# Optimization experiments

Measured on AMD Instinct MI355X. Metric: run time of the kernel, lower is better.

Reference implementation:

```python
import jax, jax.numpy as jnp
import numpy as np
import math

B, S, DIM = 1, 2048, 1024
H, KVH = 16, 4
HD = DIM // H            # 64
KV_DIM = KVH * HD        # 256


def setup_inputs() -> dict:
    key = jax.random.key(0)
    ks = jax.random.split(key, 8)
    std = 0.02
    return {
        "x": jax.random.normal(ks[0], (B, S, DIM), jnp.float32),
        "Wq": jax.random.normal(ks[1], (DIM, DIM), jnp.float32) * std,
        "Wk": jax.random.normal(ks[2], (KV_DIM, DIM), jnp.float32) * std,
        "Wv": jax.random.normal(ks[3], (KV_DIM, DIM), jnp.float32) * std,
        "Wg": jax.random.normal(ks[4], (KV_DIM, DIM), jnp.float32) * std,
        "Wo": jax.random.normal(ks[5], (DIM, DIM), jnp.float32) * std,
        "q_gain": jnp.full((H,), 1.0, jnp.float32),
        "lambda_param": jnp.full((H,), 0.5, jnp.float32),
    }


def _rms_norm(x):
    eps = jnp.finfo(x.dtype).eps
    return x * jax.lax.rsqrt(jnp.mean(x * x, axis=-1, keepdims=True) + eps)


def _polar_rotary(seq_len, head_dim, dtype):
    # PolarRotary: angles = arange(0, d, 2)/d * pi; radius decays with position
    angles = jnp.arange(0, head_dim, 2, dtype=jnp.float32) / head_dim * math.pi
    pos = jnp.arange(seq_len, dtype=jnp.float32)
    radius = 1.0 / (1.0 + pos[:, None] * 0.01)          # [S, 1]
    ang = pos[:, None] * angles[None, :]                 # [S, d/2]
    cos = (radius * jnp.cos(ang)).astype(dtype)          # [S, d/2]
    sin = (radius * jnp.sin(ang)).astype(dtype)
    return cos[None, None], sin[None, None]              # [1,1,S,d/2]


def _apply_rotary(x, cos, sin):
    half = x.shape[-1] // 2
    x1, x2 = x[..., :half], x[..., half:]
    return jnp.concatenate([x1 * cos + x2 * sin, x1 * -sin + x2 * cos], axis=-1)


def _causal_attn(q, k, v, scale, mask):
    # q,k,v: [B,H,S,d]
    s = jnp.einsum("bhqd,bhkd->bhqk", q, k) * scale
    s = jnp.where(mask, s, jnp.finfo(s.dtype).min)
    p = jax.nn.softmax(s, axis=-1)
    return jnp.einsum("bhqk,bhkd->bhqd", p, v)


def reference(x, Wq, Wk, Wv, Wg, Wo, q_gain, lambda_param):
    bsz, seqlen, dim = x.shape
    q = (x @ Wq.T).reshape(bsz, seqlen, H, HD).transpose(0, 2, 1, 3)      # [B,H,S,d]
    k = (x @ Wk.T).reshape(bsz, seqlen, KVH, HD).transpose(0, 2, 1, 3)    # [B,KVH,S,d]
    v = (x @ Wv.T).reshape(bsz, seqlen, KVH, HD).transpose(0, 2, 1, 3)

    # value gate (VGA)
    v_g = jax.nn.sigmoid((x @ Wg.T).reshape(bsz, seqlen, KVH, HD).transpose(0, 2, 1, 3))
    v = v * v_g

    q = _rms_norm(q)
    k = _rms_norm(k)

    cos, sin = _polar_rotary(seqlen, HD, q.dtype)
    q = _apply_rotary(q, cos, sin)
    k = _apply_rotary(k, cos, sin)

    q = q * q_gain.astype(q.dtype)[None, :, None, None]

    # GQA: repeat kv heads
    rep = H // KVH
    k = jnp.repeat(k, rep, axis=1)
    v = jnp.repeat(v, rep, axis=1)

    # differential attention: split head dim in halves
    half = HD // 2
    q1, q2 = q[..., :half], q[..., half:]
    k1, k2 = k[..., :half], k[..., half:]
    v1, v2 = v[..., :half], v[..., half:]

    scale = 1.0 / math.sqrt(half)
    mask = jnp.tril(jnp.ones((seqlen, seqlen), dtype=bool))[None, None]
    a1 = _causal_attn(q1, k1, v1, scale, mask)
    a2 = _causal_attn(q2, k2, v2, scale, mask)

    lp = lambda_param.astype(q.dtype)[None, :, None, None]
    y = jnp.concatenate([a1 - lp * a2, a1 + lp * a2], axis=-1)            # [B,H,S,d]
    y = y.transpose(0, 2, 1, 3).reshape(bsz, seqlen, dim)
    return y @ Wo.T
```

## Files before the change

### kernel.cpp

```cpp
#include <hip/hip_runtime.h>
#include <hip/hip_bf16.h>
#include <math.h>

#define S_LEN 2048
#define DIM   1024
#define NH    16
#define NKVH  4
#define HD    64
#define KVDIM 256

typedef __hip_bfloat16 bf16;
typedef __attribute__((ext_vector_type(8))) short short8;
typedef __attribute__((ext_vector_type(4))) float f32x4;

#define GLOBAL_AS __attribute__((address_space(1)))
#define LDS_AS    __attribute__((address_space(3)))

__device__ __forceinline__ void gload_lds16(const bf16* g, bf16* l) {
    __builtin_amdgcn_global_load_lds((const GLOBAL_AS void*)g, (LDS_AS void*)l,
                                     16, 0, 0);
}

__global__ __launch_bounds__(256) void cast6(
    const float* __restrict__ x,  const float* __restrict__ Wq,
    const float* __restrict__ Wk, const float* __restrict__ Wv,
    const float* __restrict__ Wg, const float* __restrict__ Wo,
    bf16* __restrict__ xb,  bf16* __restrict__ Wqb,
    bf16* __restrict__ Wkb, bf16* __restrict__ Wvb,
    bf16* __restrict__ Wgb, bf16* __restrict__ Wob,
    float* __restrict__ rc, float* __restrict__ rs,
    const float* __restrict__ lp) {
    if (blockIdx.y == 6) {
        const int idx = blockIdx.x * 256 + threadIdx.x;
        if (idx < S_LEN * 32) {
            const int s = idx >> 5, i = idx & 31;
            float af  = (float)(((double)(2 * i) / 64.0) * 3.14159265358979323846);
            float ang = (float)s * af;
            float radius = 1.0f / (1.0f + 0.01f * (float)s);
            rc[idx] = radius * (float)cos((double)ang);
            rs[idx] = radius * (float)sin((double)ang);
        }
        return;
    }
    if (blockIdx.y == 5) {
        for (int i = (blockIdx.x * 256 + threadIdx.x) * 4; i < DIM * DIM;
             i += gridDim.x * 1024) {
            const int n = i >> 10, c = i & (DIM - 1);
            const int h = c >> 6, half = (c >> 5) & 1, d = c & 31;
            const float* base = Wo + (size_t)n * DIM + h * 64 + d;
            float4 w1 = *(const float4*)(base);
            float4 w2 = *(const float4*)(base + 32);
            const float lam = lp[h];
            float4 r;
            if (half == 0) {
                r.x = w1.x + w2.x; r.y = w1.y + w2.y;
                r.z = w1.z + w2.z; r.w = w1.w + w2.w;
            } else {
                r.x = lam * (w2.x - w1.x); r.y = lam * (w2.y - w1.y);
                r.z = lam * (w2.z - w1.z); r.w = lam * (w2.w - w1.w);
            }
            Wob[i]     = __float2bfloat16(r.x);
            Wob[i + 1] = __float2bfloat16(r.y);
            Wob[i + 2] = __float2bfloat16(r.z);
            Wob[i + 3] = __float2bfloat16(r.w);
        }
        return;
    }
    const float* s; bf16* d; int n;
    switch (blockIdx.y) {
        case 0: s = x;  d = xb;  n = S_LEN * DIM; break;
        case 1: s = Wq; d = Wqb; n = DIM * DIM;   break;
        case 2: s = Wk; d = Wkb; n = KVDIM * DIM; break;
        case 3: s = Wv; d = Wvb; n = KVDIM * DIM; break;
        default: s = Wg; d = Wgb; n = KVDIM * DIM; break;
    }
    for (int i = (blockIdx.x * 256 + threadIdx.x) * 4; i < n; i += gridDim.x * 1024) {
        float4 v = *(const float4*)(s + i);
        d[i]     = __float2bfloat16(v.x);
        d[i + 1] = __float2bfloat16(v.y);
        d[i + 2] = __float2bfloat16(v.z);
        d[i + 3] = __float2bfloat16(v.w);
    }
}

__device__ __forceinline__ void gemm_core(
    const bf16* __restrict__ A, const bf16* __restrict__ B,
    float* __restrict__ C, int bm, int bn, int N, int K) {
    __shared__ bf16 As[64 * 64];
    __shared__ bf16 Bs[64 * 64];
    const int tid  = threadIdx.x;
    const int w    = tid >> 6;
    const int lane = tid & 63;
    const int quad = lane >> 4;
    const int lm   = lane & 15;
    const int srow = tid >> 3;
    const int sseg = (tid & 7) ^ (srow & 7);
    const bf16* a0p = A + (size_t)(bm + srow) * K + (sseg << 3);
    const bf16* a1p = a0p + (size_t)32 * K;
    const bf16* b0p = B + (size_t)(bn + srow) * K + (sseg << 3);
    const bf16* b1p = b0p + (size_t)32 * K;
    bf16* ldsA = As + w * 512;
    bf16* ldsB = Bs + w * 512;

    f32x4 acc[4] = {};
    const int ra  = w * 16 + lm;
    const int rax = ra & 7;
    const int aoff0 = ra * 64 + (((quad    ) ^ rax) << 3);
    const int aoff1 = ra * 64 + (((quad + 4) ^ rax) << 3);
    const int rbx = lm & 7;
    const int boff0 = lm * 64 + (((quad    ) ^ rbx) << 3);
    const int boff1 = lm * 64 + (((quad + 4) ^ rbx) << 3);

    for (int k0 = 0; k0 < K; k0 += 64) {
        gload_lds16(a0p + k0, ldsA);
        gload_lds16(a1p + k0, ldsA + 2048);
        gload_lds16(b0p + k0, ldsB);
        gload_lds16(b1p + k0, ldsB + 2048);
        __syncthreads();
        short8 a0 = *(const short8*)&As[aoff0];
        short8 a1 = *(const short8*)&As[aoff1];
        #pragma unroll
        for (int t = 0; t < 4; ++t) {
            short8 b0 = *(const short8*)&Bs[boff0 + t * 16 * 64];
            short8 b1 = *(const short8*)&Bs[boff1 + t * 16 * 64];
            acc[t] = __builtin_amdgcn_mfma_f32_16x16x32_bf16(a0, b0, acc[t], 0, 0, 0);
            acc[t] = __builtin_amdgcn_mfma_f32_16x16x32_bf16(a1, b1, acc[t], 0, 0, 0);
        }
        __syncthreads();
    }
    const int r0 = bm + w * 16 + quad * 4;
    #pragma unroll
    for (int t = 0; t < 4; ++t) {
        const int col = bn + t * 16 + lm;
        #pragma unroll
        for (int i = 0; i < 4; ++i)
            C[(size_t)(r0 + i) * N + col] = acc[t][i];
    }
}

__global__ __launch_bounds__(256) void gemm_out(
    const bf16* __restrict__ Yb, const bf16* __restrict__ Wob,
    float* __restrict__ C) {
    gemm_core(Yb, Wob, C, blockIdx.y * 64, blockIdx.x * 64, DIM, DIM);
}

__global__ __launch_bounds__(256) void gemm_qkvg_post(
    const bf16* __restrict__ xb,  const bf16* __restrict__ Wqb,
    const bf16* __restrict__ Wkb, const bf16* __restrict__ Wvb,
    const bf16* __restrict__ Wgb,
    bf16* __restrict__ Qb, bf16* __restrict__ Kpk, bf16* __restrict__ Vpk,
    const float* __restrict__ qgain,
    const float* __restrict__ rc, const float* __restrict__ rs) {
    __shared__ bf16 As[64 * 64];
    __shared__ bf16 Bs[64 * 64];
    __shared__ bf16 Gs[64 * 64];
    const int cx = blockIdx.x;
    const int bm = blockIdx.y * 64;
    const int tid  = threadIdx.x;
    const int w    = tid >> 6;
    const int lane = tid & 63;
    const int quad = lane >> 4;
    const int lm   = lane & 15;
    const int srow = tid >> 3;
    const int sseg = (tid & 7) ^ (srow & 7);

    int mode, bn;
    const bf16 *B0, *B1;
    if (cx < 4)      { mode = 2; bn = cx * 64;        B0 = Wvb; B1 = Wgb; }
    else if (cx < 8) { mode = 1; bn = (cx - 4) * 64;  B0 = Wkb; B1 = Wkb; }
    else             { mode = 0; bn = (cx - 8) * 64;  B0 = Wqb; B1 = Wqb; }

    const bf16* a0p = xb + (size_t)(bm + srow) * DIM + (sseg << 3);
    const bf16* a1p = a0p + (size_t)32 * DIM;
    const bf16* b0p = B0 + (size_t)(bn + srow) * DIM + (sseg << 3);
    const bf16* b1p = b0p + (size_t)32 * DIM;
    const bf16* g0p = B1 + (size_t)(bn + srow) * DIM + (sseg << 3);
    const bf16* g1p = g0p + (size_t)32 * DIM;
    bf16* ldsA = As + w * 512;
    bf16* ldsB = Bs + w * 512;
    bf16* ldsG = Gs + w * 512;

    f32x4 acc[4]  = {};
    f32x4 acc2[4] = {};
    const int ra  = w * 16 + lm;
    const int rax = ra & 7;
    const int aoff0 = ra * 64 + (((quad    ) ^ rax) << 3);
    const int aoff1 = ra * 64 + (((quad + 4) ^ rax) << 3);
    const int rbx = lm & 7;
    const int boff0 = lm * 64 + (((quad    ) ^ rbx) << 3);
    const int boff1 = lm * 64 + (((quad + 4) ^ rbx) << 3);

    for (int k0 = 0; k0 < DIM; k0 += 64) {
        gload_lds16(a0p + k0, ldsA);
        gload_lds16(a1p + k0, ldsA + 2048);
        gload_lds16(b0p + k0, ldsB);
        gload_lds16(b1p + k0, ldsB + 2048);
        if (mode == 2) {
            gload_lds16(g0p + k0, ldsG);
            gload_lds16(g1p + k0, ldsG + 2048);
        }
        __syncthreads();
        short8 a0 = *(const short8*)&As[aoff0];
        short8 a1 = *(const short8*)&As[aoff1];
        #pragma unroll
        for (int t = 0; t < 4; ++t) {
            short8 b0 = *(const short8*)&Bs[boff0 + t * 16 * 64];
            short8 b1 = *(const short8*)&Bs[boff1 + t * 16 * 64];
            acc[t] = __builtin_amdgcn_mfma_f32_16x16x32_bf16(a0, b0, acc[t], 0, 0, 0);
            acc[t] = __builtin_amdgcn_mfma_f32_16x16x32_bf16(a1, b1, acc[t], 0, 0, 0);
        }
        if (mode == 2) {
            #pragma unroll
            for (int t = 0; t < 4; ++t) {
                short8 g0 = *(const short8*)&Gs[boff0 + t * 16 * 64];
                short8 g1 = *(const short8*)&Gs[boff1 + t * 16 * 64];
                acc2[t] = __builtin_amdgcn_mfma_f32_16x16x32_bf16(a0, g0, acc2[t], 0, 0, 0);
                acc2[t] = __builtin_amdgcn_mfma_f32_16x16x32_bf16(a1, g1, acc2[t], 0, 0, 0);
            }
        }
        __syncthreads();
    }

    const int r0 = bm + w * 16 + quad * 4;
    if (mode == 2) {
        const int kvh = cx;
        #pragma unroll
        for (int t = 0; t < 4; ++t) {
            const int d = t * 16 + lm;
            const int half = d >> 5, d32 = d & 31;
            #pragma unroll
            for (int i = 0; i < 4; ++i) {
                const int s = r0 + i;
                float val = acc[t][i] / (1.0f + __expf(-acc2[t][i]));
                const size_t vi = (((((size_t)(kvh*2 + half)*64 + (s>>5))*2 + (d32>>4))*64)
                                   + ((s&31)>>3)*16 + (d32&15))*8 + (s&7);
                Vpk[vi] = __float2bfloat16(val);
            }
        }
    } else {
        const float gain = (mode == 0) ? qgain[cx - 8] : 1.0f;
        float rr[4];
        #pragma unroll
        for (int i = 0; i < 4; ++i) {
            float v0 = acc[0][i] * acc[0][i] + acc[2][i] * acc[2][i];
            float v1 = acc[1][i] * acc[1][i] + acc[3][i] * acc[3][i];
            float ssv = v0 + v1;
            ssv += __shfl_xor(ssv, 8);
            ssv += __shfl_xor(ssv, 4);
            ssv += __shfl_xor(ssv, 2);
            ssv += __shfl_xor(ssv, 1);
            rr[i] = rsqrtf(ssv * (1.0f/64.0f) + 1.1920928955078125e-7f);
        }
        #pragma unroll
        for (int t = 0; t < 4; ++t) {
            const int d = t * 16 + lm;
            #pragma unroll
            for (int i = 0; i < 4; ++i) {
                const int s = r0 + i;
                float n  = acc[t][i]     * rr[i];
                float no = acc[t ^ 2][i] * rr[i];
                const int ri = s * 32 + (d & 31);
                float c = rc[ri], sn = rs[ri];
                float val = (t < 2) ? (n * c + no * sn) * gain
                                    : (n * c + -no * sn) * gain;
                if (mode == 0) {
                    Qb[(size_t)s * DIM + (cx - 8) * 64 + d] = __float2bfloat16(val);
                } else {
                    const int kvh = cx - 4;
                    const int half = d >> 5, d32 = d & 31;
                    const size_t ki = (((((size_t)(kvh*2 + half)*64 + (s>>5))*2 + ((s&31)>>4))*64)
                                       + (d32>>3)*16 + (s&15))*8 + (d32&7);
                    Kpk[ki] = __float2bfloat16(val);
                }
            }
        }
    }
}

__global__ __launch_bounds__(256, 8) void attn_mfma(
    const bf16* __restrict__ Qb, const bf16* __restrict__ Kpk,
    const bf16* __restrict__ Vpk, bf16* __restrict__ Yab) {
    __shared__ short PW[4][640];
    __shared__ float RED[3][64][13];
    const int id    = blockIdx.x;
    const int qtile = 127 - (id >> 5);
    const int hh    = id & 31;
    const int h     = hh >> 1;
    const int half  = hh & 1;
    const int kvh   = h >> 2;
    const int tid   = threadIdx.x;
    const int wid   = tid >> 6;
    const int lane  = tid & 63;
    const int quad  = lane >> 4;
    const int m     = lane & 15;
    bf16* PWb = (bf16*)PW[wid];

    const int qrow = qtile * 16 + m;
    short8 qf = *(const short8*)(Qb + (size_t)qrow * DIM + h * HD + half * 32 + quad * 8);

    const bf16* kbase = Kpk + (size_t)(kvh * 2 + half) * 64 * 1024 + lane * 8;
    const bf16* vbase = Vpk + (size_t)(kvh * 2 + half) * 64 * 1024 + lane * 8;

    f32x4 o0 = {}, o1 = {};
    float lpart[4] = {0.f, 0.f, 0.f, 0.f};
    const float scale = 0.17677669529663687f;
    const int rbase = qtile * 16 + quad * 4;
    const int nkt = (qtile >> 1) + 1;

    for (int kb = wid; kb < nkt; kb += 4) {
        short8 kf0 = *(const short8*)(kbase + kb * 1024);
        short8 kf1 = *(const short8*)(kbase + kb * 1024 + 512);
        f32x4 s0 = {}, s1 = {};
        s0 = __builtin_amdgcn_mfma_f32_16x16x32_bf16(qf, kf0, s0, 0, 0, 0);
        s1 = __builtin_amdgcn_mfma_f32_16x16x32_bf16(qf, kf1, s1, 0, 0, 0);
        short8 vt0 = *(const short8*)(vbase + kb * 1024);
        short8 vt1 = *(const short8*)(vbase + kb * 1024 + 512);
        const int kg = kb * 32 + m;
        #pragma unroll
        for (int r = 0; r < 4; ++r) {
            const int rg = rbase + r;
            const float p0 = (kg > rg)      ? 0.f : __expf(s0[r] * scale);
            const float p1 = (kg + 16 > rg) ? 0.f : __expf(s1[r] * scale);
            lpart[r] += p0 + p1;
            PWb[(quad * 4 + r) * 40 + m]      = __float2bfloat16(p0);
            PWb[(quad * 4 + r) * 40 + 16 + m] = __float2bfloat16(p1);
        }
        asm volatile("s_waitcnt lgkmcnt(0)" ::: "memory");
        short8 pf = *(const short8*)&PW[wid][m * 40 + quad * 8];
        o0 = __builtin_amdgcn_mfma_f32_16x16x32_bf16(pf, vt0, o0, 0, 0, 0);
        o1 = __builtin_amdgcn_mfma_f32_16x16x32_bf16(pf, vt1, o1, 0, 0, 0);
    }

    if (wid > 0) {
        float* rp = &RED[wid - 1][lane][0];
        #pragma unroll
        for (int r = 0; r < 4; ++r) {
            rp[r]     = o0[r];
            rp[4 + r] = o1[r];
            rp[8 + r] = lpart[r];
        }
    }
    __syncthreads();
    if (wid == 0) {
        #pragma unroll
        for (int wv = 0; wv < 3; ++wv) {
            const float* rp = &RED[wv][lane][0];
            #pragma unroll
            for (int r = 0; r < 4; ++r) {
                o0[r]     += rp[r];
                o1[r]     += rp[4 + r];
                lpart[r]  += rp[8 + r];
            }
        }
        #pragma unroll
        for (int r = 0; r < 4; ++r) {
            float v = lpart[r];
            v += __shfl_xor(v, 1);
            v += __shfl_xor(v, 2);
            v += __shfl_xor(v, 4);
            v += __shfl_xor(v, 8);
            lpart[r] = 1.f / v;
        }
        #pragma unroll
        for (int r = 0; r < 4; ++r) {
            bf16* op = Yab + (size_t)(rbase + r) * DIM + h * HD + half * 32;
            op[m]      = __float2bfloat16(o0[r] * lpart[r]);
            op[16 + m] = __float2bfloat16(o1[r] * lpart[r]);
        }
    }
}

extern "C" void kernel_launch(void* const* d_in, const int* in_sizes, int n_in,
                              void* d_out, int out_size, void* d_ws, size_t ws_size,
                              hipStream_t stream) {
    const float* x  = (const float*)d_in[0];
    const float* Wq = (const float*)d_in[1];
    const float* Wk = (const float*)d_in[2];
    const float* Wv = (const float*)d_in[3];
    const float* Wg = (const float*)d_in[4];
    const float* Wo = (const float*)d_in[5];
    const float* qg = (const float*)d_in[6];
    const float* lp = (const float*)d_in[7];
    float* out = (float*)d_out;

    char* ws = (char*)d_ws;
    bf16* Qb   = (bf16*)ws;
    bf16* Kpk  = (bf16*)(ws + (8u << 20));
    bf16* Vpk  = (bf16*)(ws + (9u << 20));
    float* rc  = (float*)(ws + (14u << 20));
    float* rs  = (float*)(ws + (14u << 20) + (256u << 10));
    bf16* Yab  = (bf16*)(ws + (14u << 20));
    bf16* xb   = (bf16*)(ws + (22u << 20));
    bf16* Wqb  = (bf16*)(ws + (26u << 20));
    bf16* Wkb  = (bf16*)(ws + (28u << 20));
    bf16* Wvb  = (bf16*)(ws + (28u << 20) + (512u << 10));
    bf16* Wgb  = (bf16*)(ws + (29u << 20));
    bf16* Wob  = (bf16*)(ws + (29u << 20) + (512u << 10));

    cast6<<<dim3(512, 7), 256, 0, stream>>>(x, Wq, Wk, Wv, Wg, Wo,
                                            xb, Wqb, Wkb, Wvb, Wgb, Wob,
                                            rc, rs, lp);

    gemm_qkvg_post<<<dim3(24, S_LEN/64), 256, 0, stream>>>(
        xb, Wqb, Wkb, Wvb, Wgb, Qb, Kpk, Vpk, qg, rc, rs);

    attn_mfma<<<4096, 256, 0, stream>>>(Qb, Kpk, Vpk, Yab);

    gemm_out<<<dim3(DIM/64, S_LEN/64), 256, 0, stream>>>(Yab, Wob, out);
}
```

Baseline: 131.1 us.

## Double-buffer LDS tiles in projection and output GEMMs

Both the fused QKVG projection GEMM and the output GEMM now keep two LDS buffers and prefetch the next K-tile with global-to-LDS loads while MFMAs consume the current tile. Each iteration ends with a single vmcnt wait and barrier instead of two __syncthreads. The goal is to hide global memory latency behind compute. In exchange LDS use doubles, which may lower occupancy, particularly in the projection kernel with its three buffers.

Result: no change. 133.0 us (+1.5%).

```diff
diff --git a/kernel.cpp b/kernel.cpp
--- a/kernel.cpp
+++ b/kernel.cpp
@@ -19,6 +19,12 @@
 __device__ __forceinline__ void gload_lds16(const bf16* g, bf16* l) {
     __builtin_amdgcn_global_load_lds((const GLOBAL_AS void*)g, (LDS_AS void*)l,
                                      16, 0, 0);
+}
+
+__device__ __forceinline__ void wait_stage_and_barrier() {
+    asm volatile("s_waitcnt vmcnt(0)" ::: "memory");
+    __builtin_amdgcn_s_barrier();
+    asm volatile("" ::: "memory");
 }
 
 __global__ __launch_bounds__(256) void cast6(
@@ -83,11 +89,11 @@
     }
 }
 
-__device__ __forceinline__ void gemm_core(
+__device__ __forceinline__ void gemm_core_db(
     const bf16* __restrict__ A, const bf16* __restrict__ B,
     float* __restrict__ C, int bm, int bn, int N, int K) {
-    __shared__ bf16 As[64 * 64];
-    __shared__ bf16 Bs[64 * 64];
+    __shared__ bf16 As[2][64 * 64];
+    __shared__ bf16 Bs[2][64 * 64];
     const int tid  = threadIdx.x;
     const int w    = tid >> 6;
     const int lane = tid & 63;
@@ -99,8 +105,7 @@
     const bf16* a1p = a0p + (size_t)32 * K;
     const bf16* b0p = B + (size_t)(bn + srow) * K + (sseg << 3);
     const bf16* b1p = b0p + (size_t)32 * K;
-    bf16* ldsA = As + w * 512;
-    bf16* ldsB = Bs + w * 512;
+    const int wo = w * 512;
 
     f32x4 acc[4] = {};
     const int ra  = w * 16 + lm;
@@ -111,22 +116,34 @@
     const int boff0 = lm * 64 + (((quad    ) ^ rbx) << 3);
     const int boff1 = lm * 64 + (((quad + 4) ^ rbx) << 3);
 
-    for (int k0 = 0; k0 < K; k0 += 64) {
-        gload_lds16(a0p + k0, ldsA);
-        gload_lds16(a1p + k0, ldsA + 2048);
-        gload_lds16(b0p + k0, ldsB);
-        gload_lds16(b1p + k0, ldsB + 2048);
-        __syncthreads();
-        short8 a0 = *(const short8*)&As[aoff0];
-        short8 a1 = *(const short8*)&As[aoff1];
-        #pragma unroll
-        for (int t = 0; t < 4; ++t) {
-            short8 b0 = *(const short8*)&Bs[boff0 + t * 16 * 64];
-            short8 b1 = *(const short8*)&Bs[boff1 + t * 16 * 64];
-            acc[t] = __builtin_amdgcn_mfma_f32_16x16x32_bf16(a0, b0, acc[t], 0, 0, 0);
-            acc[t] = __builtin_amdgcn_mfma_f32_16x16x32_bf16(a1, b1, acc[t], 0, 0, 0);
-        }
-        __syncthreads();
+    gload_lds16(a0p, &As[0][wo]);
+    gload_lds16(a1p, &As[0][wo] + 2048);
+    gload_lds16(b0p, &Bs[0][wo]);
+    gload_lds16(b1p, &Bs[0][wo] + 2048);
+    wait_stage_and_barrier();
+
+    const int nt = K >> 6;
+    #pragma unroll 2
+    for (int t = 0; t < nt; ++t) {
+        const int cur = t & 1;
+        if (t + 1 < nt) {
+            const int k0 = (t + 1) << 6;
+            const int nb = cur ^ 1;
+            gload_lds16(a0p + k0, &As[nb][wo]);
+            gload_lds16(a1p + k0, &As[nb][wo] + 2048);
+            gload_lds16(b0p + k0, &Bs[nb][wo]);
+            gload_lds16(b1p + k0, &Bs[nb][wo] + 2048);
+        }
+        short8 a0 = *(const short8*)&As[cur][aoff0];
+        short8 a1 = *(const short8*)&As[cur][aoff1];
+        #pragma unroll
+        for (int tt = 0; tt < 4; ++tt) {
+            short8 b0 = *(const short8*)&Bs[cur][boff0 + tt * 16 * 64];
+            short8 b1 = *(const short8*)&Bs[cur][boff1 + tt * 16 * 64];
+            acc[tt] = __builtin_amdgcn_mfma_f32_16x16x32_bf16(a0, b0, acc[tt], 0, 0, 0);
+            acc[tt] = __builtin_amdgcn_mfma_f32_16x16x32_bf16(a1, b1, acc[tt], 0, 0, 0);
+        }
+        if (t + 1 < nt) wait_stage_and_barrier();
     }
     const int r0 = bm + w * 16 + quad * 4;
     #pragma unroll
@@ -141,7 +158,7 @@
 __global__ __launch_bounds__(256) void gemm_out(
     const bf16* __restrict__ Yb, const bf16* __restrict__ Wob,
     float* __restrict__ C) {
-    gemm_core(Yb, Wob, C, blockIdx.y * 64, blockIdx.x * 64, DIM, DIM);
+    gemm_core_db(Yb, Wob, C, blockIdx.y * 64, blockIdx.x * 64, DIM, DIM);
 }
 
 __global__ __launch_bounds__(256) void gemm_qkvg_post(
@@ -151,9 +168,9 @@
     bf16* __restrict__ Qb, bf16* __restrict__ Kpk, bf16* __restrict__ Vpk,
     const float* __restrict__ qgain,
     const float* __restrict__ rc, const float* __restrict__ rs) {
-    __shared__ bf16 As[64 * 64];
-    __shared__ bf16 Bs[64 * 64];
-    __shared__ bf16 Gs[64 * 64];
+    __shared__ bf16 As[2][64 * 64];
+    __shared__ bf16 Bs[2][64 * 64];
+    __shared__ bf16 Gs[2][64 * 64];
     const int cx = blockIdx.x;
     const int bm = blockIdx.y * 64;
     const int tid  = threadIdx.x;
@@ -176,9 +193,7 @@
     const bf16* b1p = b0p + (size_t)32 * DIM;
     const bf16* g0p = B1 + (size_t)(bn + srow) * DIM + (sseg << 3);
     const bf16* g1p = g0p + (size_t)32 * DIM;
-    bf16* ldsA = As + w * 512;
-    bf16* ldsB = Bs + w * 512;
-    bf16* ldsG = Gs + w * 512;
+    const int wo = w * 512;
 
     f32x4 acc[4]  = {};
     f32x4 acc2[4] = {};
@@ -190,35 +205,51 @@
     const int boff0 = lm * 64 + (((quad    ) ^ rbx) << 3);
     const int boff1 = lm * 64 + (((quad + 4) ^ rbx) << 3);
 
-    for (int k0 = 0; k0 < DIM; k0 += 64) {
-        gload_lds16(a0p + k0, ldsA);
-        gload_lds16(a1p + k0, ldsA + 2048);
-        gload_lds16(b0p + k0, ldsB);
-        gload_lds16(b1p + k0, ldsB + 2048);
-        if (mode == 2) {
-            gload_lds16(g0p + k0, ldsG);
-            gload_lds16(g1p + k0, ldsG + 2048);
-        }
-        __syncthreads();
-        short8 a0 = *(const short8*)&As[aoff0];
-        short8 a1 = *(const short8*)&As[aoff1];
-        #pragma unroll
-        for (int t = 0; t < 4; ++t) {
-            short8 b0 = *(const short8*)&Bs[boff0 + t * 16 * 64];
-            short8 b1 = *(const short8*)&Bs[boff1 + t * 16 * 64];
-            acc[t] = __builtin_amdgcn_mfma_f32_16x16x32_bf16(a0, b0, acc[t], 0, 0, 0);
-            acc[t] = __builtin_amdgcn_mfma_f32_16x16x32_bf16(a1, b1, acc[t], 0, 0, 0);
+    gload_lds16(a0p, &As[0][wo]);
+    gload_lds16(a1p, &As[0][wo] + 2048);
+    gload_lds16(b0p, &Bs[0][wo]);
+    gload_lds16(b1p, &Bs[0][wo] + 2048);
+    if (mode == 2) {
+        gload_lds16(g0p, &Gs[0][wo]);
+        gload_lds16(g1p, &Gs[0][wo] + 2048);
+    }
+    wait_stage_and_barrier();
+
+    const int nt = DIM >> 6;
+    #pragma unroll 2
+    for (int t = 0; t < nt; ++t) {
+        const int cur = t & 1;
+        if (t + 1 < nt) {
+            const int k0 = (t + 1) << 6;
+            const int nb = cur ^ 1;
+            gload_lds16(a0p + k0, &As[nb][wo]);
+            gload_lds16(a1p + k0, &As[nb][wo] + 2048);
+            gload_lds16(b0p + k0, &Bs[nb][wo]);
+            gload_lds16(b1p + k0, &Bs[nb][wo] + 2048);
+            if (mode == 2) {
+                gload_lds16(g0p + k0, &Gs[nb][wo]);
+                gload_lds16(g1p + k0, &Gs[nb][wo] + 2048);
+            }
+        }
+        short8 a0 = *(const short8*)&As[cur][aoff0];
+        short8 a1 = *(const short8*)&As[cur][aoff1];
+        #pragma unroll
+        for (int tt = 0; tt < 4; ++tt) {
+            short8 b0 = *(const short8*)&Bs[cur][boff0 + tt * 16 * 64];
+            short8 b1 = *(const short8*)&Bs[cur][boff1 + tt * 16 * 64];
+            acc[tt] = __builtin_amdgcn_mfma_f32_16x16x32_bf16(a0, b0, acc[tt], 0, 0, 0);
+            acc[tt] = __builtin_amdgcn_mfma_f32_16x16x32_bf16(a1, b1, acc[tt], 0, 0, 0);
         }
         if (mode == 2) {
             #pragma unroll
-            for (int t = 0; t < 4; ++t) {
-                short8 g0 = *(const short8*)&Gs[boff0 + t * 16 * 64];
-                short8 g1 = *(const short8*)&Gs[boff1 + t * 16 * 64];
-                acc2[t] = __builtin_amdgcn_mfma_f32_16x16x32_bf16(a0, g0, acc2[t], 0, 0, 0);
-                acc2[t] = __builtin_amdgcn_mfma_f32_16x16x32_bf16(a1, g1, acc2[t], 0, 0, 0);
-            }
-        }
-        __syncthreads();
+            for (int tt = 0; tt < 4; ++tt) {
+                short8 g0 = *(const short8*)&Gs[cur][boff0 + tt * 16 * 64];
+                short8 g1 = *(const short8*)&Gs[cur][boff1 + tt * 16 * 64];
+                acc2[tt] = __builtin_amdgcn_mfma_f32_16x16x32_bf16(a0, g0, acc2[tt], 0, 0, 0);
+                acc2[tt] = __builtin_amdgcn_mfma_f32_16x16x32_bf16(a1, g1, acc2[tt], 0, 0, 0);
+            }
+        }
+        if (t + 1 < nt) wait_stage_and_barrier();
     }
 
     const int r0 = bm + w * 16 + quad * 4;
```
